# Kernel optimization log

Measured on AMD Instinct MI355X. Metric: run time of the kernel, lower is better.

The kernel has to match this reference:

```python
import jax, jax.numpy as jnp
import numpy as np

B, S, D, H = 4, 2048, 1024, 16
DK = D // H


def setup_inputs() -> dict:
    key = jax.random.key(0)
    ks = jax.random.split(key, 12)
    s = 1.0 / np.sqrt(D)
    return {
        "query": jax.random.normal(ks[0], (B, S, D), jnp.float32),
        "key": jax.random.normal(ks[1], (B, S, D), jnp.float32),
        "value": jax.random.normal(ks[2], (B, S, D), jnp.float32),
        "mask": jnp.ones((1, 1, S, S), jnp.int32),
        "w_q": jax.random.normal(ks[3], (D, D), jnp.float32) * s,
        "b_q": jax.random.normal(ks[4], (D,), jnp.float32) * s,
        "w_k": jax.random.normal(ks[5], (D, D), jnp.float32) * s,
        "b_k": jax.random.normal(ks[6], (D,), jnp.float32) * s,
        "w_v": jax.random.normal(ks[7], (D, D), jnp.float32) * s,
        "b_v": jax.random.normal(ks[8], (D,), jnp.float32) * s,
        "w_o": jax.random.normal(ks[9], (D, D), jnp.float32) * s,
        "b_o": jax.random.normal(ks[10], (D,), jnp.float32) * s,
    }


def reference(query, key, value, mask, w_q, b_q, w_k, b_k, w_v, b_v, w_o, b_o):
    # linear projections (torch Linear: x @ W^T + b)
    q = query @ w_q.T + b_q
    k = key @ w_k.T + b_k
    v = value @ w_v.T + b_v
    # [B, S, D] -> [B, H, S, DK]
    q = q.reshape(B, S, H, DK).transpose(0, 2, 1, 3)
    k = k.reshape(B, S, H, DK).transpose(0, 2, 1, 3)
    v = v.reshape(B, S, H, DK).transpose(0, 2, 1, 3)
    scores = jnp.einsum("bhqd,bhkd->bhqk", q, k) / jnp.sqrt(jnp.float32(DK))
    scores = jnp.where(mask == 0, jnp.float32(-1e9), scores)
    attn = jax.nn.softmax(scores, axis=-1)  # dropout p=0.0 -> identity
    x = jnp.einsum("bhqk,bhkd->bhqd", attn, v)
    x = x.transpose(0, 2, 1, 3).reshape(B, S, D)
    return x @ w_o.T + b_o
```

## Files before the change

### kernel.cpp

```cpp
#include <hip/hip_runtime.h>
#include <stdint.h>

#define S_LEN 2048
#define NHEAD 16
#define DHEAD 64
#define DMODEL 1024
#define MROWS 8192

typedef unsigned short ushort_t;
typedef __attribute__((ext_vector_type(8))) __bf16 bf16x8;
typedef __attribute__((ext_vector_type(4))) float f32x4;

__device__ __forceinline__ float bf2f(ushort_t h) {
    union { unsigned int u; float f; } v; v.u = ((unsigned int)h) << 16; return v.f;
}
__device__ __forceinline__ ushort_t f2bf(float f) {
    union { float f; unsigned int u; } v; v.f = f;
    unsigned int u = v.u + 0x7fffu + ((v.u >> 16) & 1u);
    return (ushort_t)(u >> 16);
}

__device__ __forceinline__ void gload_lds16(const void* g, void* l)
{
    auto* g1 = reinterpret_cast<const __attribute__((address_space(1))) void*>(
        reinterpret_cast<uintptr_t>(g));
    auto* l3 = reinterpret_cast<__attribute__((address_space(3))) void*>(
        reinterpret_cast<uintptr_t>(l));
    __builtin_amdgcn_global_load_lds(g1, l3, 16, 0, 0);
}

__global__ void detect_dtype(const unsigned int* __restrict__ q, int* __restrict__ flag)
{
    __shared__ int cnt;
    if (threadIdx.x == 0) cnt = 0;
    __syncthreads();
    int c = 0;
    for (int i = 0; i < 8; ++i) {
        const unsigned int w = q[threadIdx.x * 8 + i];
        const unsigned int lo = w & 0xffffu;
        const unsigned int e = (lo >> 7) & 0xffu;
        if (lo == 0u || (e >= 96u && e <= 160u)) ++c;
    }
    atomicAdd(&cnt, c);
    __syncthreads();
    if (threadIdx.x == 0) flag[0] = (cnt < 400) ? 1 : 0;
}

__global__ void mask_flags(const int* __restrict__ mask, int* __restrict__ flags)
{
    __shared__ int ok_s;
    if (threadIdx.x == 0) ok_s = 1;
    __syncthreads();
    const int t = blockIdx.x;
    const int tq = t >> 4, tk = t & 15;
    int ok = 1;
    for (int i = 0; i < 64; ++i) {
        const int idx = i * 256 + threadIdx.x;
        const int r = idx >> 7, c = idx & 127;
        if (mask[(size_t)(tq * 128 + r) * S_LEN + tk * 128 + c] == 0) { ok = 0; break; }
    }
    if (!ok) atomicAnd(&ok_s, 0);
    __syncthreads();
    if (threadIdx.x == 0) flags[t] = ok_s;
}

__device__ __forceinline__ float loadscal(const void* b, int i, bool f32)
{
    return f32 ? ((const float*)b)[i] : bf2f(((const ushort_t*)b)[i]);
}

__device__ __forceinline__ void conv_body(const void* __restrict__ src,
                                          ushort_t* __restrict__ dst,
                                          int n8, bool f32)
{
    const int stride = gridDim.x * 256;
    for (int i = blockIdx.x * 256 + threadIdx.x; i < n8; i += stride) {
        if (f32) {
            const float4 a = ((const float4*)src)[2 * (size_t)i];
            const float4 b = ((const float4*)src)[2 * (size_t)i + 1];
            union { ushort_t u[8]; uint4 v; } p;
            p.u[0] = f2bf(a.x); p.u[1] = f2bf(a.y); p.u[2] = f2bf(a.z); p.u[3] = f2bf(a.w);
            p.u[4] = f2bf(b.x); p.u[5] = f2bf(b.y); p.u[6] = f2bf(b.z); p.u[7] = f2bf(b.w);
            ((uint4*)dst)[i] = p.v;
        } else {
            ((uint4*)dst)[i] = ((const uint4*)src)[i];
        }
    }
}

__global__ __launch_bounds__(256)
void conv_bf16(const void* __restrict__ src, ushort_t* __restrict__ dst,
               int n8, const int* __restrict__ dflag, int fidx)
{
    conv_body(src, dst, n8, dflag[fidx] != 0);
}

__global__ __launch_bounds__(256)
void conv_bf16_z(const void* __restrict__ s0, ushort_t* __restrict__ d0,
                 const void* __restrict__ s1, ushort_t* __restrict__ d1,
                 const void* __restrict__ s2, ushort_t* __restrict__ d2,
                 int n8, const int* __restrict__ dflag, int fidx)
{
    const int z = blockIdx.z;
    const void* src = (z == 0) ? s0 : (z == 1) ? s1 : s2;
    ushort_t*  dst = (z == 0) ? d0 : (z == 1) ? d1 : d2;
    conv_body(src, dst, n8, dflag[fidx] != 0);
}

__device__ __forceinline__ void gemm_core(
    const ushort_t* __restrict__ A, const ushort_t* __restrict__ W,
    const void* __restrict__ bias, void* __restrict__ out,
    bool bf32, bool outf, float scale,
    ushort_t (&As)[3][128 * 32], ushort_t (&Bs)[3][128 * 32])
{
    constexpr int K = DMODEL, N = DMODEL;
    const int tid = threadIdx.x;
    const int lane = tid & 63;
    const int wave = tid >> 6;
    const int lrow = lane & 15, lq = lane >> 4;
    const int m0 = blockIdx.x * 128;
    const int n0 = blockIdx.y * 128;
    const int wr = (wave >> 1) * 64;
    const int wc = (wave & 1) * 64;

    const f32x4 zero4 = {0.f, 0.f, 0.f, 0.f};
    f32x4 acc[4][4];
#pragma unroll
    for (int i = 0; i < 4; ++i)
#pragma unroll
        for (int j = 0; j < 4; ++j) acc[i][j] = zero4;

    const int r0  = tid >> 2;
    const int cc0 = (tid & 3) * 8;
    const int lb  = wave * 64 * 8;
    const int lb1 = (wave * 64 + 256) * 8;

    auto stage = [&](int buf, int k0) __attribute__((always_inline)) {
        gload_lds16(&A[(size_t)(m0 + r0) * K + k0 + cc0],      &As[buf][lb]);
        gload_lds16(&A[(size_t)(m0 + r0 + 64) * K + k0 + cc0], &As[buf][lb1]);
        gload_lds16(&W[(size_t)(n0 + r0) * K + k0 + cc0],      &Bs[buf][lb]);
        gload_lds16(&W[(size_t)(n0 + r0 + 64) * K + k0 + cc0], &Bs[buf][lb1]);
    };
    auto compute = [&](int buf) __attribute__((always_inline)) {
        bf16x8 af[4], bfr[4];
#pragma unroll
        for (int t = 0; t < 4; ++t) {
            af[t]  = *(const bf16x8*)(&As[buf][(wr + t * 16 + lrow) * 32 + lq * 8]);
            bfr[t] = *(const bf16x8*)(&Bs[buf][(wc + t * 16 + lrow) * 32 + lq * 8]);
        }
        __builtin_amdgcn_s_setprio(1);
#pragma unroll
        for (int mt = 0; mt < 4; ++mt)
#pragma unroll
            for (int nt = 0; nt < 4; ++nt)
                acc[mt][nt] = __builtin_amdgcn_mfma_f32_16x16x32_bf16(
                    af[mt], bfr[nt], acc[mt][nt], 0, 0, 0);
        __builtin_amdgcn_s_setprio(0);
    };

    stage(0, 0);
    stage(1, 32);
    asm volatile("s_waitcnt vmcnt(4)" ::: "memory");
    __builtin_amdgcn_s_barrier();

#pragma unroll 1
    for (int tt = 0; tt < 32; ++tt) {
        if (tt < 30) stage((tt + 2) % 3, (tt + 2) * 32);
        compute(tt % 3);
        if (tt < 31) {
            if (tt < 30) asm volatile("s_waitcnt vmcnt(4)" ::: "memory");
            else         asm volatile("s_waitcnt vmcnt(0)" ::: "memory");
            __builtin_amdgcn_s_barrier();
        }
    }

#pragma unroll
    for (int nt = 0; nt < 4; ++nt) {
        const int n = n0 + wc + nt * 16 + lrow;
        const float bv = loadscal(bias, n, bf32);
#pragma unroll
        for (int mt = 0; mt < 4; ++mt) {
            const int mbase = m0 + wr + mt * 16 + lq * 4;
#pragma unroll
            for (int r = 0; r < 4; ++r) {
                const float v = (acc[mt][nt][r] + bv) * scale;
                const size_t o = (size_t)(mbase + r) * N + n;
                if (outf) ((float*)out)[o] = v;
                else      ((ushort_t*)out)[o] = f2bf(v);
            }
        }
    }
}

__global__ __launch_bounds__(256, 3)
void gemm_bf16(const ushort_t* __restrict__ A, const ushort_t* __restrict__ W,
               const void* __restrict__ bias, void* __restrict__ out,
               const int* __restrict__ dflag, int outf)
{
    __shared__ ushort_t As[3][128 * 32];
    __shared__ ushort_t Bs[3][128 * 32];
    gemm_core(A, W, bias, out, dflag[1] != 0, outf != 0, 1.0f, As, Bs);
}

__global__ __launch_bounds__(256, 3)
void gemm_qk(const ushort_t* __restrict__ A0, const ushort_t* __restrict__ W0,
             const void* __restrict__ b0, void* __restrict__ o0,
             const ushort_t* __restrict__ A1, const ushort_t* __restrict__ W1,
             const void* __restrict__ b1, void* __restrict__ o1,
             const int* __restrict__ dflag)
{
    __shared__ ushort_t As[3][128 * 32];
    __shared__ ushort_t Bs[3][128 * 32];
    const bool z = blockIdx.z != 0;
    gemm_core(z ? A1 : A0, z ? W1 : W0, z ? b1 : b0, z ? o1 : o0,
              dflag[1] != 0, false, z ? 1.0f : 0.125f, As, Bs);
}

__global__ __launch_bounds__(256, 2)
void attn_mfma(const ushort_t* __restrict__ Q, const ushort_t* __restrict__ K,
               const ushort_t* __restrict__ V, const int* __restrict__ mask,
               const int* __restrict__ flags, ushort_t* __restrict__ X)
{
    constexpr int KP = 72;
    constexpr int VP = 130;
    constexpr int PP = 72;
    __shared__ ushort_t Ks[128 * KP];
    __shared__ ushort_t VTs[64 * VP];
    __shared__ ushort_t Ps[4][32 * PP];

    const int tid = threadIdx.x;
    const int lane = tid & 63;
    const int wave = tid >> 6;
    const int lrow = lane & 15, lq = lane >> 4;
    const int bh = blockIdx.y, b = bh >> 4, h = bh & 15;
    const int q0 = blockIdx.x * 128;
    const int qw = q0 + wave * 32;
    const int coff = h * 64;
    const size_t rowb = (size_t)b * S_LEN;

    bf16x8 qf[2][2];
#pragma unroll
    for (int mt = 0; mt < 2; ++mt)
#pragma unroll
        for (int ks = 0; ks < 2; ++ks)
            qf[mt][ks] = *(const bf16x8*)(
                &Q[(rowb + qw + mt * 16 + lrow) * DMODEL + coff + ks * 32 + lq * 8]);

    const f32x4 zero4 = {0.f, 0.f, 0.f, 0.f};
    f32x4 o[2][4];
    float mr[2][4], lr[2][4];
#pragma unroll
    for (int mt = 0; mt < 2; ++mt) {
#pragma unroll
        for (int nt = 0; nt < 4; ++nt) o[mt][nt] = zero4;
#pragma unroll
        for (int r = 0; r < 4; ++r) { mr[mt][r] = -1e30f; lr[mt][r] = 0.f; }
    }

    ushort_t* const pw = &Ps[wave][0];

    for (int kt = 0; kt < 16; ++kt) {
        const int k0 = kt * 128;
#pragma unroll
        for (int i = 0; i < 4; ++i) {
            const int c = tid + i * 256;
            const int r = c >> 3, cc = (c & 7) * 8;
            *(uint4*)(&Ks[r * KP + cc]) =
                *(const uint4*)(&K[(rowb + k0 + r) * DMODEL + coff + cc]);
        }
#pragma unroll
        for (int i = 0; i < 2; ++i) {
            const int c = tid + i * 256;
            const int k2 = c >> 3;
            const int cc = (c & 7) * 8;
            union { uint4 v; ushort_t u[8]; } a, bb;
            a.v  = *(const uint4*)(&V[(rowb + k0 + 2 * k2)     * DMODEL + coff + cc]);
            bb.v = *(const uint4*)(&V[(rowb + k0 + 2 * k2 + 1) * DMODEL + coff + cc]);
#pragma unroll
            for (int j = 0; j < 8; ++j) {
                const unsigned int pk = (unsigned int)a.u[j] | ((unsigned int)bb.u[j] << 16);
                *(unsigned int*)(&VTs[(cc + j) * VP + 2 * k2]) = pk;
            }
        }
        __syncthreads();

        f32x4 s[2][8];
#pragma unroll
        for (int mt = 0; mt < 2; ++mt)
#pragma unroll
            for (int nt = 0; nt < 8; ++nt) s[mt][nt] = zero4;
#pragma unroll
        for (int nt = 0; nt < 8; ++nt) {
#pragma unroll
            for (int ks = 0; ks < 2; ++ks) {
                const bf16x8 kf = *(const bf16x8*)(&Ks[(nt * 16 + lrow) * KP + ks * 32 + lq * 8]);
                s[0][nt] = __builtin_amdgcn_mfma_f32_16x16x32_bf16(qf[0][ks], kf, s[0][nt], 0, 0, 0);
                s[1][nt] = __builtin_amdgcn_mfma_f32_16x16x32_bf16(qf[1][ks], kf, s[1][nt], 0, 0, 0);
            }
        }

        if (!flags[blockIdx.x * 16 + kt]) {
            for (int mt = 0; mt < 2; ++mt)
                for (int nt = 0; nt < 8; ++nt)
                    for (int r = 0; r < 4; ++r) {
                        const int qi = qw + mt * 16 + lq * 4 + r;
                        const int ki = k0 + nt * 16 + lrow;
                        if (mask[(size_t)qi * S_LEN + ki] == 0) s[mt][nt][r] = -1e9f;
                    }
        }

#pragma unroll
        for (int mt = 0; mt < 2; ++mt) {
#pragma unroll
            for (int r = 0; r < 4; ++r) {
                float v = s[mt][0][r];
#pragma unroll
                for (int nt = 1; nt < 8; ++nt) v = fmaxf(v, s[mt][nt][r]);
#pragma unroll
                for (int off = 1; off < 16; off <<= 1) v = fmaxf(v, __shfl_xor(v, off, 64));
                const float mn = fmaxf(mr[mt][r], v);
                const float alpha = __expf(mr[mt][r] - mn);
                mr[mt][r] = mn;
                float rs = 0.f;
#pragma unroll
                for (int nt = 0; nt < 8; ++nt) {
                    const float p = __expf(s[mt][nt][r] - mn);
                    s[mt][nt][r] = p;
                    rs += p;
                }
#pragma unroll
                for (int off = 1; off < 16; off <<= 1) rs += __shfl_xor(rs, off, 64);
                lr[mt][r] = lr[mt][r] * alpha + rs;
#pragma unroll
                for (int nt = 0; nt < 4; ++nt) o[mt][nt][r] *= alpha;
            }
        }

#pragma unroll
        for (int half = 0; half < 2; ++half) {
#pragma unroll
            for (int mt = 0; mt < 2; ++mt)
#pragma unroll
                for (int nt = 0; nt < 4; ++nt)
#pragma unroll
                    for (int r = 0; r < 4; ++r)
                        pw[(mt * 16 + lq * 4 + r) * PP + nt * 16 + lrow] =
                            f2bf(s[mt][half * 4 + nt][r]);
#pragma unroll
            for (int ks = 0; ks < 2; ++ks) {
                const bf16x8 pf0 = *(const bf16x8*)(&pw[lrow * PP + ks * 32 + lq * 8]);
                const bf16x8 pf1 = *(const bf16x8*)(&pw[(16 + lrow) * PP + ks * 32 + lq * 8]);
                const int kb = half * 64 + ks * 32;
#pragma unroll
                for (int nt = 0; nt < 4; ++nt) {
                    const bf16x8 vf = *(const bf16x8*)(
                        &VTs[(nt * 16 + lrow) * VP + kb + lq * 8]);
                    o[0][nt] = __builtin_amdgcn_mfma_f32_16x16x32_bf16(pf0, vf, o[0][nt], 0, 0, 0);
                    o[1][nt] = __builtin_amdgcn_mfma_f32_16x16x32_bf16(pf1, vf, o[1][nt], 0, 0, 0);
                }
            }
        }
        __syncthreads();
    }

#pragma unroll
    for (int mt = 0; mt < 2; ++mt) {
#pragma unroll
        for (int r = 0; r < 4; ++r) {
            const float inv = 1.f / lr[mt][r];
            const int si = qw + mt * 16 + lq * 4 + r;
#pragma unroll
            for (int nt = 0; nt < 4; ++nt) {
                const int dk = nt * 16 + lrow;
                X[(rowb + si) * DMODEL + coff + dk] = f2bf(o[mt][nt][r] * inv);
            }
        }
    }
}

extern "C" void kernel_launch(void* const* d_in, const int* in_sizes, int n_in,
                              void* d_out, int out_size, void* d_ws, size_t ws_size,
                              hipStream_t stream)
{
    const void* query = d_in[0];
    const void* key   = d_in[1];
    const void* value = d_in[2];
    const int*  mask  = (const int*)d_in[3];
    const void* w_q = d_in[4];
    const void* b_q = d_in[5];
    const void* w_k = d_in[6];
    const void* b_k = d_in[7];
    const void* w_v = d_in[8];
    const void* b_v = d_in[9];
    const void* w_o = d_in[10];
    const void* b_o = d_in[11];

    const size_t TEN = (size_t)MROWS * DMODEL;
    const size_t WEL = (size_t)DMODEL * DMODEL;
    ushort_t* W0 = (ushort_t*)d_ws;
    ushort_t* W1 = W0 + TEN;
    ushort_t* W2 = W1 + TEN;
    int* dflag   = (int*)(W2 + TEN);
    int* flags   = dflag + 2;

    ushort_t* AcQ = (ushort_t*)d_out;
    ushort_t* AcK = AcQ + TEN;
    ushort_t* AcV = AcQ;
    ushort_t* Vp  = AcK;

    ushort_t* Wq_c = W2;
    ushort_t* Wk_c = W2 + WEL;
    ushort_t* Wv_c = W2 + 2 * WEL;
    ushort_t* Wo_c = W1;

    const int WN8 = (int)(WEL / 8);
    const int AN8 = (int)(TEN / 8);

    detect_dtype<<<1, 64, 0, stream>>>((const unsigned int*)query, dflag + 0);
    detect_dtype<<<1, 64, 0, stream>>>((const unsigned int*)w_q,   dflag + 1);
    mask_flags<<<256, 256, 0, stream>>>(mask, flags);

    conv_bf16_z<<<dim3(512, 1, 3), 256, 0, stream>>>(
        w_q, Wq_c, w_k, Wk_c, w_v, Wv_c, WN8, dflag, 1);
    conv_bf16_z<<<dim3(2048, 1, 2), 256, 0, stream>>>(
        query, AcQ, key, AcK, (const void*)0, (ushort_t*)0, AN8, dflag, 0);

    gemm_qk<<<dim3(64, 8, 2), 256, 0, stream>>>(AcQ, Wq_c, b_q, W0,
                                                AcK, Wk_c, b_k, W1, dflag);

    conv_bf16<<<2048, 256, 0, stream>>>(value, AcV, AN8, dflag, 0);
    gemm_bf16<<<dim3(64, 8), 256, 0, stream>>>(AcV, Wv_c, b_v, Vp, dflag, 0);

    attn_mfma<<<dim3(16, 64), 256, 0, stream>>>(W0, W1, Vp, mask, flags, W2);

    conv_bf16<<<512, 256, 0, stream>>>(w_o, Wo_c, WN8, dflag, 1);
    gemm_bf16<<<dim3(64, 8), 256, 0, stream>>>(W2, Wo_c, b_o, d_out, dflag, 1);
}
```

Baseline: 490.3 us.

## Switch projection GEMMs to 256x256 tiles with 8 waves and swizzled LDS

Replaces the 128x128, 4-wave, triple-buffered GEMM with a 256x256 tile run by 512 threads (8 waves, each computing 128x64). It uses double buffering and an XOR swizzle of the 16-byte K-chunks in LDS. The larger tile raises arithmetic intensity and data reuse per load, and the swizzle is meant to cut LDS bank conflicts. The trade-offs are fewer blocks (128 per GEMM, 256 for QK) on a GPU with many CUs, shallower prefetch that waits on vmcnt(0) every iteration, and higher register use per thread.

```diff
diff --git a/kernel.cpp b/kernel.cpp
--- a/kernel.cpp
+++ b/kernel.cpp
@@ -107,83 +107,95 @@
     conv_body(src, dst, n8, dflag[fidx] != 0);
 }
 
-__device__ __forceinline__ void gemm_core(
+__device__ __forceinline__ void gemm256_core(
     const ushort_t* __restrict__ A, const ushort_t* __restrict__ W,
     const void* __restrict__ bias, void* __restrict__ out,
     bool bf32, bool outf, float scale,
-    ushort_t (&As)[3][128 * 32], ushort_t (&Bs)[3][128 * 32])
+    ushort_t (&As)[2][256 * 32], ushort_t (&Bs)[2][256 * 32])
 {
     constexpr int K = DMODEL, N = DMODEL;
     const int tid = threadIdx.x;
     const int lane = tid & 63;
     const int wave = tid >> 6;
     const int lrow = lane & 15, lq = lane >> 4;
-    const int m0 = blockIdx.x * 128;
-    const int n0 = blockIdx.y * 128;
-    const int wr = (wave >> 1) * 64;
-    const int wc = (wave & 1) * 64;
+    const int Rw = (wave >> 2) * 128;
+    const int Cw = (wave & 3) * 64;
+    const int m0 = blockIdx.x * 256;
+    const int n0 = blockIdx.y * 256;
 
     const f32x4 zero4 = {0.f, 0.f, 0.f, 0.f};
-    f32x4 acc[4][4];
-#pragma unroll
-    for (int i = 0; i < 4; ++i)
+    f32x4 acc[8][4];
+#pragma unroll
+    for (int i = 0; i < 8; ++i)
 #pragma unroll
         for (int j = 0; j < 4; ++j) acc[i][j] = zero4;
 
-    const int r0  = tid >> 2;
-    const int cc0 = (tid & 3) * 8;
-    const int lb  = wave * 64 * 8;
-    const int lb1 = (wave * 64 + 256) * 8;
-
-    auto stage = [&](int buf, int k0) __attribute__((always_inline)) {
-        gload_lds16(&A[(size_t)(m0 + r0) * K + k0 + cc0],      &As[buf][lb]);
-        gload_lds16(&A[(size_t)(m0 + r0 + 64) * K + k0 + cc0], &As[buf][lb1]);
-        gload_lds16(&W[(size_t)(n0 + r0) * K + k0 + cc0],      &Bs[buf][lb]);
-        gload_lds16(&W[(size_t)(n0 + r0 + 64) * K + k0 + cc0], &Bs[buf][lb1]);
+    const int rowA = tid >> 2;
+    const int sl   = (((tid & 3) ^ (rowA & 3))) * 8;
+    const int lb0  = (wave * 64) * 8;
+    const int lb1  = (512 + wave * 64) * 8;
+
+    auto stage = [&](int db, int k0) __attribute__((always_inline)) {
+        gload_lds16(&A[(size_t)(m0 + rowA) * K + k0 + sl],       &As[db][lb0]);
+        gload_lds16(&A[(size_t)(m0 + rowA + 128) * K + k0 + sl], &As[db][lb1]);
+        gload_lds16(&W[(size_t)(n0 + rowA) * K + k0 + sl],       &Bs[db][lb0]);
+        gload_lds16(&W[(size_t)(n0 + rowA + 128) * K + k0 + sl], &Bs[db][lb1]);
     };
-    auto compute = [&](int buf) __attribute__((always_inline)) {
-        bf16x8 af[4], bfr[4];
-#pragma unroll
-        for (int t = 0; t < 4; ++t) {
-            af[t]  = *(const bf16x8*)(&As[buf][(wr + t * 16 + lrow) * 32 + lq * 8]);
-            bfr[t] = *(const bf16x8*)(&Bs[buf][(wc + t * 16 + lrow) * 32 + lq * 8]);
-        }
-        __builtin_amdgcn_s_setprio(1);
-#pragma unroll
-        for (int mt = 0; mt < 4; ++mt)
-#pragma unroll
-            for (int nt = 0; nt < 4; ++nt)
-                acc[mt][nt] = __builtin_amdgcn_mfma_f32_16x16x32_bf16(
-                    af[mt], bfr[nt], acc[mt][nt], 0, 0, 0);
-        __builtin_amdgcn_s_setprio(0);
-    };
+
+    const int lqs8 = (lq ^ (lrow & 3)) * 8;
 
     stage(0, 0);
-    stage(1, 32);
-    asm volatile("s_waitcnt vmcnt(4)" ::: "memory");
+    asm volatile("s_waitcnt vmcnt(0)" ::: "memory");
     __builtin_amdgcn_s_barrier();
 
 #pragma unroll 1
     for (int tt = 0; tt < 32; ++tt) {
-        if (tt < 30) stage((tt + 2) % 3, (tt + 2) * 32);
-        compute(tt % 3);
+        const int db = tt & 1;
+        if (tt < 31) stage(db ^ 1, (tt + 1) * 32);
+        const ushort_t* Ad = As[db];
+        const ushort_t* Bd = Bs[db];
+        bf16x8 bfr[4], af[4];
+#pragma unroll
+        for (int ni = 0; ni < 4; ++ni)
+            bfr[ni] = *(const bf16x8*)(&Bd[(Cw + ni * 16 + lrow) * 32 + lqs8]);
+#pragma unroll
+        for (int mi = 0; mi < 4; ++mi)
+            af[mi] = *(const bf16x8*)(&Ad[(Rw + mi * 16 + lrow) * 32 + lqs8]);
+        __builtin_amdgcn_s_setprio(1);
+#pragma unroll
+        for (int mi = 0; mi < 4; ++mi)
+#pragma unroll
+            for (int ni = 0; ni < 4; ++ni)
+                acc[mi][ni] = __builtin_amdgcn_mfma_f32_16x16x32_bf16(
+                    af[mi], bfr[ni], acc[mi][ni], 0, 0, 0);
+        __builtin_amdgcn_s_setprio(0);
+#pragma unroll
+        for (int mi = 0; mi < 4; ++mi)
+            af[mi] = *(const bf16x8*)(&Ad[(Rw + 64 + mi * 16 + lrow) * 32 + lqs8]);
+        __builtin_amdgcn_s_setprio(1);
+#pragma unroll
+        for (int mi = 0; mi < 4; ++mi)
+#pragma unroll
+            for (int ni = 0; ni < 4; ++ni)
+                acc[4 + mi][ni] = __builtin_amdgcn_mfma_f32_16x16x32_bf16(
+                    af[mi], bfr[ni], acc[4 + mi][ni], 0, 0, 0);
+        __builtin_amdgcn_s_setprio(0);
         if (tt < 31) {
-            if (tt < 30) asm volatile("s_waitcnt vmcnt(4)" ::: "memory");
-            else         asm volatile("s_waitcnt vmcnt(0)" ::: "memory");
+            asm volatile("s_waitcnt vmcnt(0)" ::: "memory");
             __builtin_amdgcn_s_barrier();
         }
     }
 
 #pragma unroll
-    for (int nt = 0; nt < 4; ++nt) {
-        const int n = n0 + wc + nt * 16 + lrow;
+    for (int ni = 0; ni < 4; ++ni) {
+        const int n = n0 + Cw + ni * 16 + lrow;
         const float bv = loadscal(bias, n, bf32);
 #pragma unroll
-        for (int mt = 0; mt < 4; ++mt) {
-            const int mbase = m0 + wr + mt * 16 + lq * 4;
+        for (int mi = 0; mi < 8; ++mi) {
+            const int mbase = m0 + Rw + (mi >> 2) * 64 + (mi & 3) * 16 + lq * 4;
 #pragma unroll
             for (int r = 0; r < 4; ++r) {
-                const float v = (acc[mt][nt][r] + bv) * scale;
+                const float v = (acc[mi][ni][r] + bv) * scale;
                 const size_t o = (size_t)(mbase + r) * N + n;
                 if (outf) ((float*)out)[o] = v;
                 else      ((ushort_t*)out)[o] = f2bf(v);
@@ -192,28 +204,28 @@
     }
 }
 
-__global__ __launch_bounds__(256, 3)
-void gemm_bf16(const ushort_t* __restrict__ A, const ushort_t* __restrict__ W,
-               const void* __restrict__ bias, void* __restrict__ out,
-               const int* __restrict__ dflag, int outf)
-{
-    __shared__ ushort_t As[3][128 * 32];
-    __shared__ ushort_t Bs[3][128 * 32];
-    gemm_core(A, W, bias, out, dflag[1] != 0, outf != 0, 1.0f, As, Bs);
-}
-
-__global__ __launch_bounds__(256, 3)
-void gemm_qk(const ushort_t* __restrict__ A0, const ushort_t* __restrict__ W0,
-             const void* __restrict__ b0, void* __restrict__ o0,
-             const ushort_t* __restrict__ A1, const ushort_t* __restrict__ W1,
-             const void* __restrict__ b1, void* __restrict__ o1,
-             const int* __restrict__ dflag)
-{
-    __shared__ ushort_t As[3][128 * 32];
-    __shared__ ushort_t Bs[3][128 * 32];
+__global__ __launch_bounds__(512, 2)
+void gemm256(const ushort_t* __restrict__ A, const ushort_t* __restrict__ W,
+             const void* __restrict__ bias, void* __restrict__ out,
+             const int* __restrict__ dflag, int outf)
+{
+    __shared__ ushort_t As[2][256 * 32];
+    __shared__ ushort_t Bs[2][256 * 32];
+    gemm256_core(A, W, bias, out, dflag[1] != 0, outf != 0, 1.0f, As, Bs);
+}
+
+__global__ __launch_bounds__(512, 2)
+void gemm256_qk(const ushort_t* __restrict__ A0, const ushort_t* __restrict__ W0,
+                const void* __restrict__ b0, void* __restrict__ o0,
+                const ushort_t* __restrict__ A1, const ushort_t* __restrict__ W1,
+                const void* __restrict__ b1, void* __restrict__ o1,
+                const int* __restrict__ dflag)
+{
+    __shared__ ushort_t As[2][256 * 32];
+    __shared__ ushort_t Bs[2][256 * 32];
     const bool z = blockIdx.z != 0;
-    gemm_core(z ? A1 : A0, z ? W1 : W0, z ? b1 : b0, z ? o1 : o0,
-              dflag[1] != 0, false, z ? 1.0f : 0.125f, As, Bs);
+    gemm256_core(z ? A1 : A0, z ? W1 : W0, z ? b1 : b0, z ? o1 : o0,
+                 dflag[1] != 0, false, z ? 1.0f : 0.125f, As, Bs);
 }
 
 __global__ __launch_bounds__(256, 2)
@@ -425,14 +437,14 @@
     conv_bf16_z<<<dim3(2048, 1, 2), 256, 0, stream>>>(
         query, AcQ, key, AcK, (const void*)0, (ushort_t*)0, AN8, dflag, 0);
 
-    gemm_qk<<<dim3(64, 8, 2), 256, 0, stream>>>(AcQ, Wq_c, b_q, W0,
-                                                AcK, Wk_c, b_k, W1, dflag);
+    gemm256_qk<<<dim3(32, 4, 2), 512, 0, stream>>>(AcQ, Wq_c, b_q, W0,
+                                                   AcK, Wk_c, b_k, W1, dflag);
 
     conv_bf16<<<2048, 256, 0, stream>>>(value, AcV, AN8, dflag, 0);
-    gemm_bf16<<<dim3(64, 8), 256, 0, stream>>>(AcV, Wv_c, b_v, Vp, dflag, 0);
+    gemm256<<<dim3(32, 4), 512, 0, stream>>>(AcV, Wv_c, b_v, Vp, dflag, 0);
 
     attn_mfma<<<dim3(16, 64), 256, 0, stream>>>(W0, W1, Vp, mask, flags, W2);
 
     conv_bf16<<<512, 256, 0, stream>>>(w_o, Wo_c, WN8, dflag, 1);
-    gemm_bf16<<<dim3(64, 8), 256, 0, stream>>>(W2, Wo_c, b_o, d_out, dflag, 1);
-}
+    gemm256<<<dim3(32, 4), 512, 0, stream>>>(W2, Wo_c, b_o, d_out, dflag, 1);
+}
```

Result: slower. 514.7 us (+5.0%).
